# Optimization experiments

Hardware: AMD Instinct MI355X
Metric: run time of the kernel (lower is better)

The kernel has to match this reference:

```python
import jax, jax.numpy as jnp
import numpy as np

FILLUP = -100  # SentimentClasses.FILLUP_POLARITY_VALUE
SMOOTHING = 0.2
B, C, T = 2097152, 3, 5


def setup_inputs() -> dict:
    key = jax.random.key(0)
    k1, k2, k3 = jax.random.split(key, 3)
    predictions = jax.random.normal(k1, (B, C, T), dtype=jnp.float32)
    labels = jax.random.randint(k2, (B, T), 0, C, dtype=jnp.int64)
    fill_mask = jax.random.uniform(k3, (B, T)) < 0.1
    labels = jnp.where(fill_mask, jnp.asarray(FILLUP, labels.dtype), labels)
    return {"predictions": predictions, "labels": labels}


def reference(predictions, labels):
    # predictions: [B, C, T], labels: [B, T]
    num_classes = predictions.shape[1]
    log_probs = jax.nn.log_softmax(predictions, axis=1)  # [B, C, T]

    base_prob = SMOOTHING / num_classes
    valid = labels != FILLUP                              # [B, T]
    safe_labels = jnp.where(valid, labels, 0)
    # one-hot over class axis -> [B, C, T]
    one_hot = jax.nn.one_hot(safe_labels, num_classes, axis=1, dtype=log_probs.dtype)
    smooth = base_prob + (1.0 - SMOOTHING) * one_hot * valid[:, None, :]
    # mask out fillup targets entirely (base_prob included)
    smooth = smooth * valid[:, None, :].astype(log_probs.dtype)

    loss = jnp.sum(-smooth * log_probs, axis=(1, 2))      # [B]
    return jnp.mean(loss)
```

## Files before the change

kernel.cpp:

```cpp
#include <hip/hip_runtime.h>


constexpr int   FILLUP  = -100;
constexpr float BASEP   = 0.2f / 3.0f;
constexpr float CONF    = 0.8f;
constexpr int   NB      = 2097152;
constexpr int   THREADS = 256;
constexpr int   ROWS    = 512;
constexpr int   NBLOCKS = NB / ROWS;
constexpr int   PRED_F4 = ROWS * 15 / 4;
constexpr int   LAB_I4  = ROWS * 5 / 4;

__global__ __launch_bounds__(THREADS)
void ce_lsr_stage1(const float4* __restrict__ pred4,
                   const int4*  __restrict__ lab4,
                   float* __restrict__ partial) {
    __shared__ __align__(16) float predS[ROWS * 15];
    __shared__ __align__(16) int   labS[ROWS * 5];

    const int t = threadIdx.x;
    const size_t pbase = (size_t)blockIdx.x * PRED_F4;
    const size_t lbase = (size_t)blockIdx.x * LAB_I4;

    float4* predS4 = reinterpret_cast<float4*>(predS);
#pragma unroll
    for (int i = 0; i < 8; ++i) {
        const int idx = i * THREADS + t;
        if (idx < PRED_F4) predS4[idx] = pred4[pbase + idx];
    }
    int4* labS4 = reinterpret_cast<int4*>(labS);
#pragma unroll
    for (int i = 0; i < 3; ++i) {
        const int idx = i * THREADS + t;
        if (idx < LAB_I4) labS4[idx] = lab4[lbase + idx];
    }
    __syncthreads();

    float acc = 0.0f;
#pragma unroll
    for (int rr = 0; rr < 2; ++rr) {
        const int r = t + rr * THREADS;
        const float* __restrict__ xr = &predS[r * 15];
        const int*   __restrict__ lr = &labS[r * 5];
#pragma unroll
        for (int tt = 0; tt < 5; ++tt) {
            const int   l  = lr[tt];
            const float x0 = xr[tt];
            const float x1 = xr[5 + tt];
            const float x2 = xr[10 + tt];
            const float m   = fmaxf(fmaxf(x0, x1), x2);
            const float s   = __expf(x0 - m) + __expf(x1 - m) + __expf(x2 - m);
            const float lse = m + __logf(s);
            const float xl  = (l == 1) ? x1 : ((l == 2) ? x2 : x0);
            const float c   = lse - BASEP * (x0 + x1 + x2) - CONF * xl;
            acc += (l != FILLUP) ? c : 0.0f;
        }
    }

#pragma unroll
    for (int off = 32; off > 0; off >>= 1)
        acc += __shfl_down(acc, off, 64);

    __shared__ float wsum[THREADS / 64];
    const int lane = t & 63;
    const int wid  = t >> 6;
    if (lane == 0) wsum[wid] = acc;
    __syncthreads();
    if (t == 0) {
        float s = 0.0f;
#pragma unroll
        for (int w = 0; w < THREADS / 64; ++w) s += wsum[w];
        partial[blockIdx.x] = s;
    }
}

__global__ __launch_bounds__(256)
void ce_lsr_stage2(const float* __restrict__ partial,
                   float* __restrict__ out) {
    float acc = 0.0f;
#pragma unroll
    for (int i = 0; i < NBLOCKS / 256; ++i)
        acc += partial[i * 256 + threadIdx.x];
#pragma unroll
    for (int off = 32; off > 0; off >>= 1)
        acc += __shfl_down(acc, off, 64);

    __shared__ float wsum[4];
    const int lane = threadIdx.x & 63;
    const int wid  = threadIdx.x >> 6;
    if (lane == 0) wsum[wid] = acc;
    __syncthreads();
    if (threadIdx.x == 0) {
        const float s = wsum[0] + wsum[1] + wsum[2] + wsum[3];
        out[0] = s * (1.0f / (float)NB);
    }
}

extern "C" void kernel_launch(void* const* d_in, const int* in_sizes, int n_in,
                              void* d_out, int out_size, void* d_ws, size_t ws_size,
                              hipStream_t stream) {
    const float4* pred4 = (const float4*)d_in[0];
    const int4*   lab4  = (const int4*)d_in[1];
    float* out     = (float*)d_out;
    float* partial = (float*)d_ws;

    ce_lsr_stage1<<<NBLOCKS, THREADS, 0, stream>>>(pred4, lab4, partial);
    ce_lsr_stage2<<<1, 256, 0, stream>>>(partial, out);
}
```

Before: 37.84 us.

## Double-buffer row chunks via direct global-to-LDS loads in persistent blocks

After: 33.19 us. 12.3% less time.

```diff
diff --git a/kernel.cpp b/kernel.cpp
--- a/kernel.cpp
+++ b/kernel.cpp
@@ -1,4 +1,5 @@
 #include <hip/hip_runtime.h>
+#include <stdint.h>
 
 
 constexpr int   FILLUP  = -100;
@@ -6,42 +7,60 @@
 constexpr float CONF    = 0.8f;
 constexpr int   NB      = 2097152;
 constexpr int   THREADS = 256;
-constexpr int   ROWS    = 512;
-constexpr int   NBLOCKS = NB / ROWS;
-constexpr int   PRED_F4 = ROWS * 15 / 4;
-constexpr int   LAB_I4  = ROWS * 5 / 4;
+constexpr int   CROWS   = 256;
+constexpr int   NCHUNK  = NB / CROWS;
+constexpr int   CPB     = 8;
+constexpr int   NBLOCKS = NCHUNK / CPB;
+constexpr int   PRED_CB = CROWS * 15 * 4;
+constexpr int   LAB_CB  = CROWS * 5 * 4;
+constexpr int   PRED_SLOTS = PRED_CB / 16;
+constexpr int   LAB_SLOTS  = LAB_CB / 16;
+
+__device__ __forceinline__ void gll16(const void* g, void* l) {
+    __builtin_amdgcn_global_load_lds(
+        (const __attribute__((address_space(1))) void*)g,
+        (__attribute__((address_space(3))) void*)l, 16, 0, 0);
+}
+
+__device__ __forceinline__ void stage_chunk(const char* __restrict__ predB,
+                                            const char* __restrict__ labB,
+                                            int chunk, char* predL, char* labL,
+                                            int t) {
+    const char* ps = predB + (size_t)chunk * PRED_CB;
+    const char* ls = labB  + (size_t)chunk * LAB_CB;
+#pragma unroll
+    for (int i = 0; i < 4; ++i) {
+        const int idx = i * THREADS + t;
+        if (idx < PRED_SLOTS) gll16(ps + (size_t)idx * 16, predL + idx * 16);
+    }
+#pragma unroll
+    for (int i = 0; i < 2; ++i) {
+        const int idx = i * THREADS + t;
+        if (idx < LAB_SLOTS) gll16(ls + (size_t)idx * 16, labL + idx * 16);
+    }
+}
 
 __global__ __launch_bounds__(THREADS)
-void ce_lsr_stage1(const float4* __restrict__ pred4,
-                   const int4*  __restrict__ lab4,
+void ce_lsr_stage1(const char* __restrict__ predB,
+                   const char* __restrict__ labB,
                    float* __restrict__ partial) {
-    __shared__ __align__(16) float predS[ROWS * 15];
-    __shared__ __align__(16) int   labS[ROWS * 5];
+    __shared__ __align__(16) char predS[2][PRED_CB];
+    __shared__ __align__(16) char labS[2][LAB_CB];
 
     const int t = threadIdx.x;
-    const size_t pbase = (size_t)blockIdx.x * PRED_F4;
-    const size_t lbase = (size_t)blockIdx.x * LAB_I4;
+    const int cbase = blockIdx.x * CPB;
 
-    float4* predS4 = reinterpret_cast<float4*>(predS);
-#pragma unroll
-    for (int i = 0; i < 8; ++i) {
-        const int idx = i * THREADS + t;
-        if (idx < PRED_F4) predS4[idx] = pred4[pbase + idx];
-    }
-    int4* labS4 = reinterpret_cast<int4*>(labS);
-#pragma unroll
-    for (int i = 0; i < 3; ++i) {
-        const int idx = i * THREADS + t;
-        if (idx < LAB_I4) labS4[idx] = lab4[lbase + idx];
-    }
+    stage_chunk(predB, labB, cbase, predS[0], labS[0], t);
     __syncthreads();
 
     float acc = 0.0f;
-#pragma unroll
-    for (int rr = 0; rr < 2; ++rr) {
-        const int r = t + rr * THREADS;
-        const float* __restrict__ xr = &predS[r * 15];
-        const int*   __restrict__ lr = &labS[r * 5];
+    for (int k = 0; k < CPB; ++k) {
+        const int cur = k & 1;
+        if (k + 1 < CPB)
+            stage_chunk(predB, labB, cbase + k + 1, predS[cur ^ 1], labS[cur ^ 1], t);
+
+        const float* __restrict__ xr = (const float*)(predS[cur]) + t * 15;
+        const int*   __restrict__ lr = (const int*)(labS[cur]) + t * 5;
 #pragma unroll
         for (int tt = 0; tt < 5; ++tt) {
             const int   l  = lr[tt];
@@ -55,23 +74,18 @@
             const float c   = lse - BASEP * (x0 + x1 + x2) - CONF * xl;
             acc += (l != FILLUP) ? c : 0.0f;
         }
+        __syncthreads();
     }
 
 #pragma unroll
     for (int off = 32; off > 0; off >>= 1)
         acc += __shfl_down(acc, off, 64);
 
-    __shared__ float wsum[THREADS / 64];
-    const int lane = t & 63;
-    const int wid  = t >> 6;
-    if (lane == 0) wsum[wid] = acc;
+    float* wsum = (float*)predS;
+    if ((t & 63) == 0) wsum[t >> 6] = acc;
     __syncthreads();
-    if (t == 0) {
-        float s = 0.0f;
-#pragma unroll
-        for (int w = 0; w < THREADS / 64; ++w) s += wsum[w];
-        partial[blockIdx.x] = s;
-    }
+    if (t == 0)
+        partial[blockIdx.x] = wsum[0] + wsum[1] + wsum[2] + wsum[3];
 }
 
 __global__ __launch_bounds__(256)
@@ -99,11 +113,11 @@
 extern "C" void kernel_launch(void* const* d_in, const int* in_sizes, int n_in,
                               void* d_out, int out_size, void* d_ws, size_t ws_size,
                               hipStream_t stream) {
-    const float4* pred4 = (const float4*)d_in[0];
-    const int4*   lab4  = (const int4*)d_in[1];
+    const char* pred = (const char*)d_in[0];
+    const char* lab  = (const char*)d_in[1];
     float* out     = (float*)d_out;
     float* partial = (float*)d_ws;
 
-    ce_lsr_stage1<<<NBLOCKS, THREADS, 0, stream>>>(pred4, lab4, partial);
+    ce_lsr_stage1<<<NBLOCKS, THREADS, 0, stream>>>(pred, lab, partial);
     ce_lsr_stage2<<<1, 256, 0, stream>>>(partial, out);
 }
```
